# Performance work log

Hardware: AMD Instinct MI355X
Metric: run time of the kernel (lower is better)

The kernel has to match this reference:

```python
import jax, jax.numpy as jnp
import numpy as np

B, N, D, H = 2, 2048, 1024, 16
DH = D // H
DF = 4 * D
SCALE = D ** (-0.5)  # standard_scale=False -> dim**-0.5
EPS = 1e-5


def _ln(x, w, b):
    mu = jnp.mean(x, axis=-1, keepdims=True)
    var = jnp.mean(jnp.square(x - mu), axis=-1, keepdims=True)
    return (x - mu) * jax.lax.rsqrt(var + EPS) * w + b


def setup_inputs() -> dict:
    key = jax.random.key(0)
    ks = jax.random.split(key, 12)
    s = lambda fan_in: (1.0 / np.sqrt(fan_in))
    return {
        "x": jax.random.normal(ks[0], (B, N, D), jnp.float32),
        "gamma": jax.random.uniform(ks[1], (B, H), jnp.float32),
        "dist_matrix": jax.random.uniform(ks[2], (N, N), jnp.float32),
        "ln1_w": jnp.ones((D,), jnp.float32),
        "ln1_b": jnp.zeros((D,), jnp.float32),
        "qkv_w": jax.random.normal(ks[3], (D, 3 * D), jnp.float32) * s(D),
        "qkv_b": jnp.zeros((3 * D,), jnp.float32),
        "proj_w": jax.random.normal(ks[4], (D, D), jnp.float32) * s(D),
        "proj_b": jnp.zeros((D,), jnp.float32),
        "ln2_w": jnp.ones((D,), jnp.float32),
        "ln2_b": jnp.zeros((D,), jnp.float32),
        "mlp_w1": jax.random.normal(ks[5], (D, DF), jnp.float32) * s(D),
        "mlp_b1": jnp.zeros((DF,), jnp.float32),
        "mlp_w2": jax.random.normal(ks[6], (DF, D), jnp.float32) * s(DF),
        "mlp_b2": jnp.zeros((D,), jnp.float32),
    }


def reference(x, gamma, dist_matrix, ln1_w, ln1_b, qkv_w, qkv_b, proj_w, proj_b,
              ln2_w, ln2_b, mlp_w1, mlp_b1, mlp_w2, mlp_b2):
    # --- ZoomAttention on norm1(x) ---
    h = _ln(x, ln1_w, ln1_b)                                   # [B,N,D]
    qkv = h @ qkv_w + qkv_b                                    # [B,N,3D]
    qkv = qkv.reshape(B, N, 3, H, DH).transpose(2, 0, 3, 1, 4)  # [3,B,H,N,DH]
    q, k, v = qkv[0], qkv[1], qkv[2]
    scores = jnp.einsum("bhnd,bhmd->bhnm", q, k) * SCALE       # [B,H,N,N]
    scores = scores - gamma[:, :, None, None] * dist_matrix[None, None]
    attn = jax.nn.softmax(scores, axis=-1)
    out = jnp.einsum("bhnm,bhmd->bhnd", attn, v)               # [B,H,N,DH]
    out = out.transpose(0, 2, 1, 3).reshape(B, N, D)
    x = x + (out @ proj_w + proj_b)
    # --- MLP (exact GELU, torch default) ---
    h2 = _ln(x, ln2_w, ln2_b)
    h2 = jax.nn.gelu(h2 @ mlp_w1 + mlp_b1, approximate=False) @ mlp_w2 + mlp_b2
    return x + h2
```

## Files before the change

### kernel.cpp

```cpp
#include <hip/hip_runtime.h>
#include <hip/hip_bf16.h>


#define SCALE_ 0.03125f
#define EPS_   1e-5f
#define LOG2E_ 1.4426950408889634f
#define SC2_   (SCALE_ * LOG2E_)

typedef unsigned short u16;
typedef __attribute__((ext_vector_type(8))) short short8;
typedef __attribute__((ext_vector_type(4))) float f32x4;
typedef __attribute__((ext_vector_type(4))) unsigned short u16x4;

__device__ inline float b2f(u16 u){ unsigned x = ((unsigned)u) << 16; float f; __builtin_memcpy(&f, &x, 4); return f; }
__device__ inline u16 f2b(float f){ __hip_bfloat16 h = __float2bfloat16(f); u16 u; __builtin_memcpy(&u, &h, 2); return u; }

__device__ inline void glds16(const u16* g, u16* l) {
    __builtin_amdgcn_global_load_lds(
        (const __attribute__((address_space(1))) void*)g,
        (__attribute__((address_space(3))) void*)l, 16, 0, 0);
}

__global__ __launch_bounds__(256) void transpose_cast(const float* __restrict__ src,
                                                      u16* __restrict__ dst, int K, int N) {
    __shared__ float t[32][33];
    int nb = blockIdx.x * 32, kb = blockIdx.y * 32;
    int tx = threadIdx.x & 31, ty = threadIdx.x >> 5;
    for (int i = 0; i < 4; i++) {
        int r = ty + i * 8;
        t[r][tx] = src[(size_t)(kb + r) * N + nb + tx];
    }
    __syncthreads();
    for (int i = 0; i < 4; i++) {
        int r = ty + i * 8;
        dst[(size_t)(nb + r) * K + kb + tx] = f2b(t[tx][r]);
    }
}

__global__ __launch_bounds__(256) void ln_bf16(const float* __restrict__ x,
                                               const float* __restrict__ w,
                                               const float* __restrict__ b,
                                               u16* __restrict__ out) {
    int row = blockIdx.x, t = threadIdx.x;
    float4 v = ((const float4*)(x + (size_t)row * 1024))[t];
    float s1 = v.x + v.y + v.z + v.w;
    float s2 = v.x * v.x + v.y * v.y + v.z * v.z + v.w * v.w;
    for (int o = 32; o > 0; o >>= 1) { s1 += __shfl_xor(s1, o); s2 += __shfl_xor(s2, o); }
    __shared__ float a1[4], a2[4];
    if ((t & 63) == 0) { a1[t >> 6] = s1; a2[t >> 6] = s2; }
    __syncthreads();
    s1 = a1[0] + a1[1] + a1[2] + a1[3];
    s2 = a2[0] + a2[1] + a2[2] + a2[3];
    float mu = s1 * (1.0f / 1024.0f);
    float var = s2 * (1.0f / 1024.0f) - mu * mu;
    float rs = rsqrtf(var + EPS_);
    float4 wv = ((const float4*)w)[t];
    float4 bv = ((const float4*)b)[t];
    u16x4 o;
    o[0] = f2b((v.x - mu) * rs * wv.x + bv.x);
    o[1] = f2b((v.y - mu) * rs * wv.y + bv.y);
    o[2] = f2b((v.z - mu) * rs * wv.z + bv.z);
    o[3] = f2b((v.w - mu) * rs * wv.w + bv.w);
    ((u16x4*)(out + (size_t)row * 1024))[t] = o;
}

template <int MODE>
__global__ __launch_bounds__(512) void gemm256_8ph(
    const u16* __restrict__ A, const u16* __restrict__ Bt,
    const float* __restrict__ bias, int K,
    u16* __restrict__ outb,
    u16* __restrict__ qp, u16* __restrict__ kp, u16* __restrict__ vtp) {
    __shared__ u16 LS[4][2][256 * 32];
    int tid = threadIdx.x;
    int w = tid >> 6, lane = tid & 63, g = lane >> 4, ln = lane & 15;
    int wr = w >> 2, wc = w & 3;
    int gx = gridDim.x;
    int nwg = gx * gridDim.y;
    int lin = blockIdx.y * gx + blockIdx.x;
    int swz = (lin & 7) * (nwg >> 3) + (lin >> 3);
    int bx = swz % gx, by = swz / gx;
    int br = by * 256, bc = bx * 256;
    int jx = (((lane & 3) ^ ((lane >> 3) & 3)) << 3);
    const u16* Ast = A + (size_t)(br + w * 32 + (lane >> 2)) * K + jx;
    const u16* Bst = Bt + (size_t)(bc + w * 32 + (lane >> 2)) * K + jx;
    size_t r16 = (size_t)16 * K;
    const int ldsW = (w * 32) * 32;
    f32x4 acc[8][4] = {};
    int NT = K >> 5;
    int slotr = ((g ^ ((ln >> 1) & 3)) << 3);
    for (int kt = 0; kt < 3; ++kt) {
        glds16(Ast + (size_t)kt * 32, &LS[kt][0][ldsW]);
        glds16(Ast + (size_t)kt * 32 + r16, &LS[kt][0][ldsW + 512]);
        glds16(Bst + (size_t)kt * 32, &LS[kt][1][ldsW]);
        glds16(Bst + (size_t)kt * 32 + r16, &LS[kt][1][ldsW + 512]);
    }
    asm volatile("s_waitcnt vmcnt(8)" ::: "memory");
    __builtin_amdgcn_s_barrier();
    short8 aa[4], bb[4];
    for (int kt = 0; kt < NT; ++kt) {
        const u16* bufA = &LS[kt & 3][0][0];
        const u16* bufB = &LS[kt & 3][1][0];
        int s3 = kt + 3;
        #pragma unroll
        for (int m = 0; m < 4; ++m)
            aa[m] = *(const short8*)&bufA[(wr * 128 + m * 16 + ln) * 32 + slotr];
        #pragma unroll
        for (int n = 0; n < 4; ++n)
            bb[n] = *(const short8*)&bufB[(wc * 64 + n * 16 + ln) * 32 + slotr];
        if (s3 < NT) {
            u16* d = &LS[s3 & 3][0][ldsW];
            glds16(Ast + (size_t)s3 * 32, d);
            glds16(Ast + (size_t)s3 * 32 + r16, d + 512);
        }
        __builtin_amdgcn_s_barrier();
        asm volatile("s_waitcnt lgkmcnt(0)" ::: "memory");
        __builtin_amdgcn_sched_barrier(0);
        __builtin_amdgcn_s_setprio(1);
        #pragma unroll
        for (int m = 0; m < 4; ++m)
            #pragma unroll
            for (int n = 0; n < 4; ++n)
                acc[m][n] = __builtin_amdgcn_mfma_f32_16x16x32_bf16(aa[m], bb[n], acc[m][n], 0, 0, 0);
        __builtin_amdgcn_s_setprio(0);
        __builtin_amdgcn_sched_barrier(0);
        __builtin_amdgcn_s_barrier();
        #pragma unroll
        for (int m = 0; m < 4; ++m)
            aa[m] = *(const short8*)&bufA[(wr * 128 + 64 + m * 16 + ln) * 32 + slotr];
        if (s3 < NT) {
            u16* d = &LS[s3 & 3][1][ldsW];
            glds16(Bst + (size_t)s3 * 32, d);
            glds16(Bst + (size_t)s3 * 32 + r16, d + 512);
        }
        if (kt + 3 < NT)      asm volatile("s_waitcnt vmcnt(8)" ::: "memory");
        else if (kt + 2 < NT) asm volatile("s_waitcnt vmcnt(4)" ::: "memory");
        else if (kt + 1 < NT) asm volatile("s_waitcnt vmcnt(0)" ::: "memory");
        __builtin_amdgcn_s_barrier();
        asm volatile("s_waitcnt lgkmcnt(0)" ::: "memory");
        __builtin_amdgcn_sched_barrier(0);
        __builtin_amdgcn_s_setprio(1);
        #pragma unroll
        for (int m = 0; m < 4; ++m)
            #pragma unroll
            for (int n = 0; n < 4; ++n)
                acc[4 + m][n] = __builtin_amdgcn_mfma_f32_16x16x32_bf16(aa[m], bb[n], acc[4 + m][n], 0, 0, 0);
        __builtin_amdgcn_s_setprio(0);
        __builtin_amdgcn_sched_barrier(0);
        __builtin_amdgcn_s_barrier();
    }
    #pragma unroll
    for (int m = 0; m < 8; ++m) {
        int row0 = br + wr * 128 + m * 16 + g * 4;
        #pragma unroll
        for (int n = 0; n < 4; ++n) {
            int col = bc + wc * 64 + n * 16 + ln;
            float bv = bias[col];
            if constexpr (MODE == 0) {
                int which = col >> 10, cc = col & 1023, hh = cc >> 6, dh = cc & 63;
                int bb2 = row0 >> 11, nn0 = row0 & 2047;
                size_t bh = (size_t)(bb2 * 16 + hh);
                if (which == 0) {
                    for (int r = 0; r < 4; r++)
                        qp[((bh * 2048 + nn0 + r) << 6) + dh] = f2b((acc[m][n][r] + bv) * SC2_);
                } else if (which == 1) {
                    for (int r = 0; r < 4; r++)
                        kp[((bh * 2048 + nn0 + r) << 6) + dh] = f2b(acc[m][n][r] + bv);
                } else {
                    u16x4 o;
                    for (int r = 0; r < 4; r++) o[r] = f2b(acc[m][n][r] + bv);
                    *(u16x4*)&vtp[((bh * 64 + dh) << 11) + nn0] = o;
                }
            } else {
                for (int r = 0; r < 4; r++) {
                    float v = acc[m][n][r] + bv;
                    float gl = 0.5f * v * (1.0f + erff(v * 0.7071067811865476f));
                    outb[(size_t)(row0 + r) * 4096 + col] = f2b(gl);
                }
            }
        }
    }
}

template <int MODE, int BN>
__global__ __launch_bounds__(256) void gemm_bf16(
    const u16* __restrict__ A, const u16* __restrict__ Bt,
    const float* __restrict__ bias, int M, int N, int K,
    const float* __restrict__ res, float* __restrict__ outf) {
    constexpr int NN = BN / 32;
    __shared__ u16 As[128 * 64];
    __shared__ u16 Bs[BN * 64];
    int br = blockIdx.y * 128, bc = blockIdx.x * BN;
    int tid = threadIdx.x;
    int w = tid >> 6, lane = tid & 63, g = lane >> 4, ln = lane & 15;
    int wr = (w >> 1) * 64, wc = (w & 1) * (BN / 2);
    f32x4 acc[4][NN] = {};
    int sgcol = (((lane & 7) ^ (lane >> 3)) << 3);
    int arow = w * 32 + (lane >> 3);
    int brow = w * (BN / 4) + (lane >> 3);
    const u16* Ap = A + (size_t)(br + arow) * K + sgcol;
    const u16* Bp = Bt + (size_t)(bc + brow) * K + sgcol;
    u16* lA = &As[(w * 32) * 64];
    u16* lB = &Bs[(w * (BN / 4)) * 64];
    size_t rstep = (size_t)8 * K;
    for (int kt = 0; kt < K; kt += 64) {
        __syncthreads();
        #pragma unroll
        for (int i = 0; i < 4; i++) glds16(Ap + kt + i * rstep, lA + i * 512);
        #pragma unroll
        for (int i = 0; i < BN / 32; i++) glds16(Bp + kt + i * rstep, lB + i * 512);
        __syncthreads();
        #pragma unroll
        for (int kk = 0; kk < 2; kk++) {
            int so = (((kk << 2) + g) ^ (ln & 7)) << 3;
            short8 af[4], bfr[NN];
            #pragma unroll
            for (int m = 0; m < 4; m++)  af[m]  = *(const short8*)&As[(wr + m * 16 + ln) * 64 + so];
            #pragma unroll
            for (int n = 0; n < NN; n++) bfr[n] = *(const short8*)&Bs[(wc + n * 16 + ln) * 64 + so];
            #pragma unroll
            for (int m = 0; m < 4; m++)
                #pragma unroll
                for (int n = 0; n < NN; n++)
                    acc[m][n] = __builtin_amdgcn_mfma_f32_16x16x32_bf16(af[m], bfr[n], acc[m][n], 0, 0, 0);
        }
    }
    #pragma unroll
    for (int m = 0; m < 4; m++) {
        int row0 = br + wr + m * 16 + g * 4;
        #pragma unroll
        for (int n = 0; n < NN; n++) {
            int col = bc + wc + n * 16 + ln;
            float bv = bias[col];
            if constexpr (MODE == 1) {
                for (int r = 0; r < 4; r++) {
                    size_t idx = (size_t)(row0 + r) * 1024 + col;
                    outf[idx] = res[idx] + acc[m][n][r] + bv;
                }
            } else {
                for (int r = 0; r < 4; r++) {
                    size_t idx = (size_t)(row0 + r) * 1024 + col;
                    outf[idx] = outf[idx] + acc[m][n][r] + bv;
                }
            }
        }
    }
}

__global__ __launch_bounds__(256) void attn_fwd(
    const u16* __restrict__ qg, const u16* __restrict__ kg, const u16* __restrict__ vtg,
    const float* __restrict__ dist, const float* __restrict__ gamma, u16* __restrict__ ao) {
    __shared__ u16 Ks[2][64 * 64];
    __shared__ u16 Vs[2][64 * 64];
    __shared__ u16 Ps[4][16 * 64];
    int qt = blockIdx.x, bh = blockIdx.y;
    int b = bh >> 4, h = bh & 15;
    int tid = threadIdx.x, w = tid >> 6, lane = tid & 63, g = lane >> 4, ln = lane & 15;
    float gam2 = gamma[bh] * LOG2E_;
    int qglob = qt * 64 + w * 16 + ln;
    const u16* qrow = qg + ((size_t)bh * 2048 + qglob) * 64;
    short8 qf0 = *(const short8*)(qrow + g * 8);
    short8 qf1 = *(const short8*)(qrow + 32 + g * 8);
    const float* dbase = dist + (size_t)qglob * 2048 + g * 4;
    float m2 = -3.0e38f;
    f32x4 acco[4] = {};
    f32x4 accl = {};
    short8 ones;
    #pragma unroll
    for (int i = 0; i < 8; ++i) ones[i] = (short)0x3F80;
    int srow = tid >> 2, sc = (tid & 3) * 2;
    int ss0 = ((sc ^ (srow & 7)) << 3), ss1 = (((sc + 1) ^ (srow & 7)) << 3);
    const u16* kgp = kg + ((size_t)bh * 2048 + srow) * 64 + sc * 8;
    const u16* vgp = vtg + ((size_t)bh * 64 + srow) * 2048 + sc * 8;
    {
        short8 a0 = *(const short8*)(kgp);
        short8 a1 = *(const short8*)(kgp + 8);
        short8 c0 = *(const short8*)(vgp);
        short8 c1 = *(const short8*)(vgp + 8);
        *(short8*)&Ks[0][srow * 64 + ss0] = a0;
        *(short8*)&Ks[0][srow * 64 + ss1] = a1;
        *(short8*)&Vs[0][srow * 64 + ss0] = c0;
        *(short8*)&Vs[0][srow * 64 + ss1] = c1;
    }
    float4 dcv[4];
    #pragma unroll
    for (int nb = 0; nb < 4; nb++) dcv[nb] = *(const float4*)(dbase + nb * 16);
    __syncthreads();
    int cur = 0;
    int so0 = (g ^ (ln & 7)) << 3, so1 = ((4 + g) ^ (ln & 7)) << 3;
    for (int kt = 0; kt < 32; kt++) {
        short8 kr0, kr1, vr0, vr1;
        float4 dnx[4];
        if (kt < 31) {
            kr0 = *(const short8*)(kgp + (kt + 1) * 4096);
            kr1 = *(const short8*)(kgp + (kt + 1) * 4096 + 8);
            vr0 = *(const short8*)(vgp + (kt + 1) * 64);
            vr1 = *(const short8*)(vgp + (kt + 1) * 64 + 8);
            #pragma unroll
            for (int nb = 0; nb < 4; nb++)
                dnx[nb] = *(const float4*)(dbase + (kt + 1) * 64 + nb * 16);
        }
        f32x4 sa[4] = {};
        __builtin_amdgcn_s_setprio(1);
        #pragma unroll
        for (int nb = 0; nb < 4; nb++) {
            short8 kf0 = *(const short8*)&Ks[cur][(nb * 16 + ln) * 64 + so0];
            short8 kf1 = *(const short8*)&Ks[cur][(nb * 16 + ln) * 64 + so1];
            sa[nb] = __builtin_amdgcn_mfma_f32_16x16x32_bf16(kf0, qf0, sa[nb], 0, 0, 0);
            sa[nb] = __builtin_amdgcn_mfma_f32_16x16x32_bf16(kf1, qf1, sa[nb], 0, 0, 0);
        }
        __builtin_amdgcn_s_setprio(0);
        float sv[4][4], pm = -3.0e38f;
        #pragma unroll
        for (int nb = 0; nb < 4; nb++) {
            float4 dv = dcv[nb];
            sv[nb][0] = sa[nb][0] - gam2 * dv.x;
            sv[nb][1] = sa[nb][1] - gam2 * dv.y;
            sv[nb][2] = sa[nb][2] - gam2 * dv.z;
            sv[nb][3] = sa[nb][3] - gam2 * dv.w;
            #pragma unroll
            for (int r = 0; r < 4; r++) pm = fmaxf(pm, sv[nb][r]);
        }
        pm = fmaxf(pm, __shfl_xor(pm, 16));
        pm = fmaxf(pm, __shfl_xor(pm, 32));
        if (!__all(pm - m2 <= 8.0f)) {
            float nm = fmaxf(m2, pm);
            float al = __builtin_exp2f(m2 - nm);
            m2 = nm;
            accl *= al;
            #pragma unroll
            for (int db = 0; db < 4; db++) acco[db] *= al;
        }
        #pragma unroll
        for (int nb = 0; nb < 4; nb++) {
            u16x4 pw;
            #pragma unroll
            for (int r = 0; r < 4; r++) pw[r] = f2b(__builtin_exp2f(sv[nb][r] - m2));
            int off = nb * 16 + g * 4;
            *(u16x4*)&Ps[w][ln * 64 + (((off >> 3) ^ (ln & 7)) << 3) + (off & 7)] = pw;
        }
        short8 pf0 = *(const short8*)&Ps[w][ln * 64 + so0];
        short8 pf1 = *(const short8*)&Ps[w][ln * 64 + so1];
        __builtin_amdgcn_s_setprio(1);
        #pragma unroll
        for (int db = 0; db < 4; db++) {
            short8 vf0 = *(const short8*)&Vs[cur][(db * 16 + ln) * 64 + so0];
            short8 vf1 = *(const short8*)&Vs[cur][(db * 16 + ln) * 64 + so1];
            acco[db] = __builtin_amdgcn_mfma_f32_16x16x32_bf16(vf0, pf0, acco[db], 0, 0, 0);
            acco[db] = __builtin_amdgcn_mfma_f32_16x16x32_bf16(vf1, pf1, acco[db], 0, 0, 0);
        }
        accl = __builtin_amdgcn_mfma_f32_16x16x32_bf16(ones, pf0, accl, 0, 0, 0);
        accl = __builtin_amdgcn_mfma_f32_16x16x32_bf16(ones, pf1, accl, 0, 0, 0);
        __builtin_amdgcn_s_setprio(0);
        if (kt < 31) {
            int nx = cur ^ 1;
            *(short8*)&Ks[nx][srow * 64 + ss0] = kr0;
            *(short8*)&Ks[nx][srow * 64 + ss1] = kr1;
            *(short8*)&Vs[nx][srow * 64 + ss0] = vr0;
            *(short8*)&Vs[nx][srow * 64 + ss1] = vr1;
            #pragma unroll
            for (int nb = 0; nb < 4; nb++) dcv[nb] = dnx[nb];
            __syncthreads();
            cur = nx;
        }
    }
    float inv = 1.0f / accl[0];
    u16* aop = ao + (size_t)(b * 2048 + qglob) * 1024 + h * 64 + g * 4;
    #pragma unroll
    for (int db = 0; db < 4; db++) {
        u16x4 o;
        #pragma unroll
        for (int r = 0; r < 4; r++) o[r] = f2b(acco[db][r] * inv);
        *(u16x4*)(aop + db * 16) = o;
    }
}

extern "C" void kernel_launch(void* const* d_in, const int* in_sizes, int n_in,
                              void* d_out, int out_size, void* d_ws, size_t ws_size,
                              hipStream_t stream) {
    const float* x     = (const float*)d_in[0];
    const float* gamma = (const float*)d_in[1];
    const float* dist  = (const float*)d_in[2];
    const float* ln1w  = (const float*)d_in[3];
    const float* ln1b  = (const float*)d_in[4];
    const float* qkvw  = (const float*)d_in[5];
    const float* qkvb  = (const float*)d_in[6];
    const float* projw = (const float*)d_in[7];
    const float* projb = (const float*)d_in[8];
    const float* ln2w  = (const float*)d_in[9];
    const float* ln2b  = (const float*)d_in[10];
    const float* w1    = (const float*)d_in[11];
    const float* b1    = (const float*)d_in[12];
    const float* w2    = (const float*)d_in[13];
    const float* b2    = (const float*)d_in[14];
    float* out = (float*)d_out;
    char* ws = (char*)d_ws;
    u16* wqkvT  = (u16*)(ws + 0);
    u16* wprojT = (u16*)(ws + 6291456);
    u16* w1T    = (u16*)(ws + 8388608);
    u16* w2T    = (u16*)(ws + 16777216);
    u16* hb     = (u16*)(ws + 33554432);
    u16* qb     = (u16*)(ws + 41943040);
    u16* kb     = (u16*)(ws + 50331648);
    u16* vtb    = (u16*)(ws + 58720256);
    u16* aob    = (u16*)(ws + 67108864);
    u16* gb     = hb;
    u16* h2b    = aob;

    dim3 blk(256);
    transpose_cast<<<dim3(3072 / 32, 1024 / 32), blk, 0, stream>>>(qkvw, wqkvT, 1024, 3072);
    transpose_cast<<<dim3(1024 / 32, 1024 / 32), blk, 0, stream>>>(projw, wprojT, 1024, 1024);
    transpose_cast<<<dim3(4096 / 32, 1024 / 32), blk, 0, stream>>>(w1, w1T, 1024, 4096);
    transpose_cast<<<dim3(1024 / 32, 4096 / 32), blk, 0, stream>>>(w2, w2T, 4096, 1024);
    ln_bf16<<<4096, blk, 0, stream>>>(x, ln1w, ln1b, hb);
    gemm256_8ph<0><<<dim3(12, 16), dim3(512), 0, stream>>>(hb, wqkvT, qkvb, 1024,
                                                           nullptr, qb, kb, vtb);
    attn_fwd<<<dim3(32, 32), blk, 0, stream>>>(qb, kb, vtb, dist, gamma, aob);
    gemm_bf16<1, 64><<<dim3(16, 32), blk, 0, stream>>>(aob, wprojT, projb, 4096, 1024, 1024,
                                                       x, out);
    ln_bf16<<<4096, blk, 0, stream>>>(out, ln2w, ln2b, h2b);
    gemm256_8ph<2><<<dim3(16, 16), dim3(512), 0, stream>>>(h2b, w1T, b1, 1024,
                                                           gb, nullptr, nullptr, nullptr);
    gemm_bf16<3, 64><<<dim3(16, 32), blk, 0, stream>>>(gb, w2T, b2, 4096, 1024, 4096,
                                                       nullptr, out);
}
```

Measured before the change: 297.2 us.

## Rewrite attention with 32x32 MFMA, register-resident P, async LDS loads, bf16 dist

The attention kernel now gives each wave 32 query rows and uses 32x32x16 bf16 MFMA instead of 16x16x32. The softmax probabilities stay in registers, repacked with cvt_pk_bf16 and permlane32_swap, so the LDS round trip through Ps and the ones-MFMA row sum are gone. The row sum is accumulated in scalar registers instead. K and V tiles are copied with global_load_lds straight into shared memory rather than staged through registers. A new pre-pass casts the distance matrix to bf16 with log2e folded in, halving the per-tile distance traffic at the cost of an extra kernel and lower precision in the bias term.

```diff
diff --git a/kernel.cpp b/kernel.cpp
--- a/kernel.cpp
+++ b/kernel.cpp
@@ -10,6 +10,7 @@
 typedef unsigned short u16;
 typedef __attribute__((ext_vector_type(8))) short short8;
 typedef __attribute__((ext_vector_type(4))) float f32x4;
+typedef __attribute__((ext_vector_type(16))) float f32x16;
 typedef __attribute__((ext_vector_type(4))) unsigned short u16x4;
 
 __device__ inline float b2f(u16 u){ unsigned x = ((unsigned)u) << 16; float f; __builtin_memcpy(&f, &x, 4); return f; }
@@ -19,6 +20,20 @@
     __builtin_amdgcn_global_load_lds(
         (const __attribute__((address_space(1))) void*)g,
         (__attribute__((address_space(3))) void*)l, 16, 0, 0);
+}
+
+__device__ inline unsigned cvtpk(float a, float b) {
+    unsigned r;
+    asm("v_cvt_pk_bf16_f32 %0, %1, %2" : "=v"(r) : "v"(a), "v"(b));
+    return r;
+}
+__device__ inline void pl32swap(unsigned &a, unsigned &b) {
+    asm("v_permlane32_swap_b32 %0, %1" : "+v"(a), "+v"(b));
+}
+__device__ inline short8 mk8(unsigned a, unsigned b, unsigned c, unsigned d) {
+    union { unsigned u[4]; short8 s; } x;
+    x.u[0] = a; x.u[1] = b; x.u[2] = c; x.u[3] = d;
+    return x.s;
 }
 
 __global__ __launch_bounds__(256) void transpose_cast(const float* __restrict__ src,
@@ -34,6 +49,18 @@
     for (int i = 0; i < 4; i++) {
         int r = ty + i * 8;
         dst[(size_t)(nb + r) * K + kb + tx] = f2b(t[tx][r]);
+    }
+}
+
+__global__ __launch_bounds__(256) void cast_scale_bf16(const float* __restrict__ src,
+                                                       u16* __restrict__ dst, int n4, float scale) {
+    int i = blockIdx.x * 256 + threadIdx.x;
+    if (i < n4) {
+        float4 v = ((const float4*)src)[i];
+        u16x4 o;
+        o[0] = f2b(v.x * scale); o[1] = f2b(v.y * scale);
+        o[2] = f2b(v.z * scale); o[3] = f2b(v.w * scale);
+        ((u16x4*)dst)[i] = o;
     }
 }
 
@@ -246,131 +273,126 @@
     }
 }
 
-__global__ __launch_bounds__(256) void attn_fwd(
+__global__ __launch_bounds__(256) void attn_fwd32(
     const u16* __restrict__ qg, const u16* __restrict__ kg, const u16* __restrict__ vtg,
-    const float* __restrict__ dist, const float* __restrict__ gamma, u16* __restrict__ ao) {
+    const u16* __restrict__ distb, const float* __restrict__ gamma, u16* __restrict__ ao) {
     __shared__ u16 Ks[2][64 * 64];
     __shared__ u16 Vs[2][64 * 64];
-    __shared__ u16 Ps[4][16 * 64];
     int qt = blockIdx.x, bh = blockIdx.y;
-    int b = bh >> 4, h = bh & 15;
-    int tid = threadIdx.x, w = tid >> 6, lane = tid & 63, g = lane >> 4, ln = lane & 15;
-    float gam2 = gamma[bh] * LOG2E_;
-    int qglob = qt * 64 + w * 16 + ln;
+    int b = bh >> 4, h16 = bh & 15;
+    int tid = threadIdx.x, w = tid >> 6, lane = tid & 63;
+    int ln = lane & 31, hh = lane >> 5;
+    float gam = gamma[bh];
+    int qglob = qt * 128 + w * 32 + ln;
     const u16* qrow = qg + ((size_t)bh * 2048 + qglob) * 64;
-    short8 qf0 = *(const short8*)(qrow + g * 8);
-    short8 qf1 = *(const short8*)(qrow + 32 + g * 8);
-    const float* dbase = dist + (size_t)qglob * 2048 + g * 4;
-    float m2 = -3.0e38f;
-    f32x4 acco[4] = {};
-    f32x4 accl = {};
-    short8 ones;
+    short8 qB[4];
     #pragma unroll
-    for (int i = 0; i < 8; ++i) ones[i] = (short)0x3F80;
-    int srow = tid >> 2, sc = (tid & 3) * 2;
-    int ss0 = ((sc ^ (srow & 7)) << 3), ss1 = (((sc + 1) ^ (srow & 7)) << 3);
-    const u16* kgp = kg + ((size_t)bh * 2048 + srow) * 64 + sc * 8;
-    const u16* vgp = vtg + ((size_t)bh * 64 + srow) * 2048 + sc * 8;
-    {
-        short8 a0 = *(const short8*)(kgp);
-        short8 a1 = *(const short8*)(kgp + 8);
-        short8 c0 = *(const short8*)(vgp);
-        short8 c1 = *(const short8*)(vgp + 8);
-        *(short8*)&Ks[0][srow * 64 + ss0] = a0;
-        *(short8*)&Ks[0][srow * 64 + ss1] = a1;
-        *(short8*)&Vs[0][srow * 64 + ss0] = c0;
-        *(short8*)&Vs[0][srow * 64 + ss1] = c1;
-    }
-    float4 dcv[4];
-    #pragma unroll
-    for (int nb = 0; nb < 4; nb++) dcv[nb] = *(const float4*)(dbase + nb * 16);
+    for (int st = 0; st < 4; ++st) qB[st] = *(const short8*)(qrow + st * 16 + hh * 8);
+    const u16* drow = distb + (size_t)qglob * 2048 + hh * 4;
+    int srow = w * 16 + (lane >> 3);
+    int sgc = (((lane & 7) ^ ((lane >> 3) & 7)) << 3);
+    const u16* kst = kg + ((size_t)bh * 2048 + srow) * 64 + sgc;
+    const u16* vst = vtg + ((size_t)bh * 64 + srow) * 2048 + sgc;
+    u16* lk0 = &Ks[0][(w * 16) * 64]; u16* lk1 = &Ks[1][(w * 16) * 64];
+    u16* lv0 = &Vs[0][(w * 16) * 64]; u16* lv1 = &Vs[1][(w * 16) * 64];
+    glds16(kst, lk0); glds16(kst + 512, lk0 + 512);
+    glds16(vst, lv0); glds16(vst + 16384, lv0 + 512);
     __syncthreads();
+    float m2 = -3.0e38f, lsum = 0.0f;
+    f32x16 acc0 = {}, acc1 = {};
     int cur = 0;
-    int so0 = (g ^ (ln & 7)) << 3, so1 = ((4 + g) ^ (ln & 7)) << 3;
-    for (int kt = 0; kt < 32; kt++) {
-        short8 kr0, kr1, vr0, vr1;
-        float4 dnx[4];
+    for (int kt = 0; kt < 32; ++kt) {
         if (kt < 31) {
-            kr0 = *(const short8*)(kgp + (kt + 1) * 4096);
-            kr1 = *(const short8*)(kgp + (kt + 1) * 4096 + 8);
-            vr0 = *(const short8*)(vgp + (kt + 1) * 64);
-            vr1 = *(const short8*)(vgp + (kt + 1) * 64 + 8);
-            #pragma unroll
-            for (int nb = 0; nb < 4; nb++)
-                dnx[nb] = *(const float4*)(dbase + (kt + 1) * 64 + nb * 16);
-        }
-        f32x4 sa[4] = {};
+            u16* dk = cur ? lk0 : lk1;
+            u16* dvp = cur ? lv0 : lv1;
+            const u16* ks = kst + (size_t)(kt + 1) * 4096;
+            const u16* vs = vst + (size_t)(kt + 1) * 64;
+            glds16(ks, dk); glds16(ks + 512, dk + 512);
+            glds16(vs, dvp); glds16(vs + 16384, dvp + 512);
+        }
+        u16x4 dd[8];
+        #pragma unroll
+        for (int i = 0; i < 8; ++i)
+            dd[i] = *(const u16x4*)(drow + kt * 64 + (i >> 2) * 32 + (i & 3) * 8);
+        const u16* KB = &Ks[cur][0];
+        const u16* VB = &Vs[cur][0];
+        f32x16 sa0 = {}, sa1 = {};
         __builtin_amdgcn_s_setprio(1);
         #pragma unroll
-        for (int nb = 0; nb < 4; nb++) {
-            short8 kf0 = *(const short8*)&Ks[cur][(nb * 16 + ln) * 64 + so0];
-            short8 kf1 = *(const short8*)&Ks[cur][(nb * 16 + ln) * 64 + so1];
-            sa[nb] = __builtin_amdgcn_mfma_f32_16x16x32_bf16(kf0, qf0, sa[nb], 0, 0, 0);
-            sa[nb] = __builtin_amdgcn_mfma_f32_16x16x32_bf16(kf1, qf1, sa[nb], 0, 0, 0);
+        for (int st = 0; st < 4; ++st) {
+            int so = (((st * 2 + hh) ^ (ln & 7)) << 3);
+            short8 kf0 = *(const short8*)&KB[ln * 64 + so];
+            short8 kf1 = *(const short8*)&KB[(32 + ln) * 64 + so];
+            sa0 = __builtin_amdgcn_mfma_f32_32x32x16_bf16(kf0, qB[st], sa0, 0, 0, 0);
+            sa1 = __builtin_amdgcn_mfma_f32_32x32x16_bf16(kf1, qB[st], sa1, 0, 0, 0);
         }
         __builtin_amdgcn_s_setprio(0);
-        float sv[4][4], pm = -3.0e38f;
-        #pragma unroll
-        for (int nb = 0; nb < 4; nb++) {
-            float4 dv = dcv[nb];
-            sv[nb][0] = sa[nb][0] - gam2 * dv.x;
-            sv[nb][1] = sa[nb][1] - gam2 * dv.y;
-            sv[nb][2] = sa[nb][2] - gam2 * dv.z;
-            sv[nb][3] = sa[nb][3] - gam2 * dv.w;
-            #pragma unroll
-            for (int r = 0; r < 4; r++) pm = fmaxf(pm, sv[nb][r]);
-        }
-        pm = fmaxf(pm, __shfl_xor(pm, 16));
+        float p0[16], p1[16];
+        float pm = -3.0e38f;
+        #pragma unroll
+        for (int r = 0; r < 16; ++r) {
+            p0[r] = sa0[r] - gam * b2f(dd[r >> 2][r & 3]);
+            p1[r] = sa1[r] - gam * b2f(dd[4 + (r >> 2)][r & 3]);
+            pm = fmaxf(pm, fmaxf(p0[r], p1[r]));
+        }
         pm = fmaxf(pm, __shfl_xor(pm, 32));
         if (!__all(pm - m2 <= 8.0f)) {
             float nm = fmaxf(m2, pm);
             float al = __builtin_exp2f(m2 - nm);
             m2 = nm;
-            accl *= al;
-            #pragma unroll
-            for (int db = 0; db < 4; db++) acco[db] *= al;
-        }
-        #pragma unroll
-        for (int nb = 0; nb < 4; nb++) {
-            u16x4 pw;
-            #pragma unroll
-            for (int r = 0; r < 4; r++) pw[r] = f2b(__builtin_exp2f(sv[nb][r] - m2));
-            int off = nb * 16 + g * 4;
-            *(u16x4*)&Ps[w][ln * 64 + (((off >> 3) ^ (ln & 7)) << 3) + (off & 7)] = pw;
-        }
-        short8 pf0 = *(const short8*)&Ps[w][ln * 64 + so0];
-        short8 pf1 = *(const short8*)&Ps[w][ln * 64 + so1];
+            lsum *= al;
+            acc0 *= al; acc1 *= al;
+        }
+        float ps = 0.0f;
+        #pragma unroll
+        for (int r = 0; r < 16; ++r) {
+            p0[r] = __builtin_exp2f(p0[r] - m2); ps += p0[r];
+            p1[r] = __builtin_exp2f(p1[r] - m2); ps += p1[r];
+        }
+        lsum += ps;
+        unsigned w0[8], w1[8];
+        #pragma unroll
+        for (int qr = 0; qr < 4; ++qr) {
+            w0[qr * 2]     = cvtpk(p0[qr * 4], p0[qr * 4 + 1]);
+            w0[qr * 2 + 1] = cvtpk(p0[qr * 4 + 2], p0[qr * 4 + 3]);
+            w1[qr * 2]     = cvtpk(p1[qr * 4], p1[qr * 4 + 1]);
+            w1[qr * 2 + 1] = cvtpk(p1[qr * 4 + 2], p1[qr * 4 + 3]);
+        }
+        pl32swap(w0[0], w0[2]); pl32swap(w0[1], w0[3]);
+        pl32swap(w0[4], w0[6]); pl32swap(w0[5], w0[7]);
+        pl32swap(w1[0], w1[2]); pl32swap(w1[1], w1[3]);
+        pl32swap(w1[4], w1[6]); pl32swap(w1[5], w1[7]);
+        short8 pB[4];
+        pB[0] = mk8(w0[0], w0[1], w0[2], w0[3]);
+        pB[1] = mk8(w0[4], w0[5], w0[6], w0[7]);
+        pB[2] = mk8(w1[0], w1[1], w1[2], w1[3]);
+        pB[3] = mk8(w1[4], w1[5], w1[6], w1[7]);
         __builtin_amdgcn_s_setprio(1);
         #pragma unroll
-        for (int db = 0; db < 4; db++) {
-            short8 vf0 = *(const short8*)&Vs[cur][(db * 16 + ln) * 64 + so0];
-            short8 vf1 = *(const short8*)&Vs[cur][(db * 16 + ln) * 64 + so1];
-            acco[db] = __builtin_amdgcn_mfma_f32_16x16x32_bf16(vf0, pf0, acco[db], 0, 0, 0);
-            acco[db] = __builtin_amdgcn_mfma_f32_16x16x32_bf16(vf1, pf1, acco[db], 0, 0, 0);
-        }
-        accl = __builtin_amdgcn_mfma_f32_16x16x32_bf16(ones, pf0, accl, 0, 0, 0);
-        accl = __builtin_amdgcn_mfma_f32_16x16x32_bf16(ones, pf1, accl, 0, 0, 0);
+        for (int sg = 0; sg < 4; ++sg) {
+            int so = (((sg * 2 + hh) ^ (ln & 7)) << 3);
+            short8 vf0 = *(const short8*)&VB[ln * 64 + so];
+            short8 vf1 = *(const short8*)&VB[(32 + ln) * 64 + so];
+            acc0 = __builtin_amdgcn_mfma_f32_32x32x16_bf16(vf0, pB[sg], acc0, 0, 0, 0);
+            acc1 = __builtin_amdgcn_mfma_f32_32x32x16_bf16(vf1, pB[sg], acc1, 0, 0, 0);
+        }
         __builtin_amdgcn_s_setprio(0);
-        if (kt < 31) {
-            int nx = cur ^ 1;
-            *(short8*)&Ks[nx][srow * 64 + ss0] = kr0;
-            *(short8*)&Ks[nx][srow * 64 + ss1] = kr1;
-            *(short8*)&Vs[nx][srow * 64 + ss0] = vr0;
-            *(short8*)&Vs[nx][srow * 64 + ss1] = vr1;
-            #pragma unroll
-            for (int nb = 0; nb < 4; nb++) dcv[nb] = dnx[nb];
-            __syncthreads();
-            cur = nx;
-        }
-    }
-    float inv = 1.0f / accl[0];
-    u16* aop = ao + (size_t)(b * 2048 + qglob) * 1024 + h * 64 + g * 4;
+        __syncthreads();
+        cur ^= 1;
+    }
+    lsum += __shfl_xor(lsum, 32);
+    float inv = 1.0f / lsum;
+    u16* aop = ao + ((size_t)(b * 2048 + qglob)) * 1024 + h16 * 64 + hh * 4;
     #pragma unroll
-    for (int db = 0; db < 4; db++) {
-        u16x4 o;
-        #pragma unroll
-        for (int r = 0; r < 4; r++) o[r] = f2b(acco[db][r] * inv);
-        *(u16x4*)(aop + db * 16) = o;
+    for (int qr = 0; qr < 4; ++qr) {
+        u16x4 o0, o1;
+        #pragma unroll
+        for (int r = 0; r < 4; ++r) {
+            o0[r] = f2b(acc0[qr * 4 + r] * inv);
+            o1[r] = f2b(acc1[qr * 4 + r] * inv);
+        }
+        *(u16x4*)(aop + qr * 8) = o0;
+        *(u16x4*)(aop + 32 + qr * 8) = o1;
     }
 }
 
@@ -398,6 +420,7 @@
     u16* wprojT = (u16*)(ws + 6291456);
     u16* w1T    = (u16*)(ws + 8388608);
     u16* w2T    = (u16*)(ws + 16777216);
+    u16* distb  = (u16*)(ws + 25165824);
     u16* hb     = (u16*)(ws + 33554432);
     u16* qb     = (u16*)(ws + 41943040);
     u16* kb     = (u16*)(ws + 50331648);
@@ -411,10 +434,11 @@
     transpose_cast<<<dim3(1024 / 32, 1024 / 32), blk, 0, stream>>>(projw, wprojT, 1024, 1024);
     transpose_cast<<<dim3(4096 / 32, 1024 / 32), blk, 0, stream>>>(w1, w1T, 1024, 4096);
     transpose_cast<<<dim3(1024 / 32, 4096 / 32), blk, 0, stream>>>(w2, w2T, 4096, 1024);
+    cast_scale_bf16<<<4096, blk, 0, stream>>>(dist, distb, 2048 * 2048 / 4, LOG2E_);
     ln_bf16<<<4096, blk, 0, stream>>>(x, ln1w, ln1b, hb);
     gemm256_8ph<0><<<dim3(12, 16), dim3(512), 0, stream>>>(hb, wqkvT, qkvb, 1024,
                                                            nullptr, qb, kb, vtb);
-    attn_fwd<<<dim3(32, 32), blk, 0, stream>>>(qb, kb, vtb, dist, gamma, aob);
+    attn_fwd32<<<dim3(16, 32), blk, 0, stream>>>(qb, kb, vtb, distb, gamma, aob);
     gemm_bf16<1, 64><<<dim3(16, 32), blk, 0, stream>>>(aob, wprojT, projb, 4096, 1024, 1024,
                                                        x, out);
     ln_bf16<<<4096, blk, 0, stream>>>(out, ln2w, ln2b, h2b);
```

New measurement: 304.4 us. 2.4% more time.

## Cast dist matrix to bf16, widen attention blocks, sum softmax denominator in VALU

Applied to the files above, without the earlier changes.

The distance matrix is pre-cast to bf16 with log2e folded in, so the attention kernel reads half the bytes per score tile. The attention block grows to 512 threads covering 128 query rows, which halves how often K/V tiles are loaded per query. The row-sum now uses VALU adds and shuffles instead of extra MFMAs with a ones vector, and a packed bf16 conversion instruction is used. Rounding dist to bf16 adds approximation error to the bias term, and the extra cast kernel costs a full pass over the 16MB matrix.

```diff
diff --git a/kernel.cpp b/kernel.cpp
--- a/kernel.cpp
+++ b/kernel.cpp
@@ -19,6 +19,12 @@
     __builtin_amdgcn_global_load_lds(
         (const __attribute__((address_space(1))) void*)g,
         (__attribute__((address_space(3))) void*)l, 16, 0, 0);
+}
+
+__device__ inline unsigned cvtpk(float a, float b) {
+    unsigned r;
+    asm("v_cvt_pk_bf16_f32 %0, %1, %2" : "=v"(r) : "v"(a), "v"(b));
+    return r;
 }
 
 __global__ __launch_bounds__(256) void transpose_cast(const float* __restrict__ src,
@@ -34,6 +40,18 @@
     for (int i = 0; i < 4; i++) {
         int r = ty + i * 8;
         dst[(size_t)(nb + r) * K + kb + tx] = f2b(t[tx][r]);
+    }
+}
+
+__global__ __launch_bounds__(256) void cast_scale_bf16(const float* __restrict__ src,
+                                                       u16* __restrict__ dst, int n4, float scale) {
+    int i = blockIdx.x * 256 + threadIdx.x;
+    if (i < n4) {
+        float4 v = ((const float4*)src)[i];
+        u16x4 o;
+        o[0] = f2b(v.x * scale); o[1] = f2b(v.y * scale);
+        o[2] = f2b(v.z * scale); o[3] = f2b(v.w * scale);
+        ((u16x4*)dst)[i] = o;
     }
 }
 
@@ -246,58 +264,48 @@
     }
 }
 
-__global__ __launch_bounds__(256) void attn_fwd(
+__global__ __launch_bounds__(512) void attn_fwd(
     const u16* __restrict__ qg, const u16* __restrict__ kg, const u16* __restrict__ vtg,
-    const float* __restrict__ dist, const float* __restrict__ gamma, u16* __restrict__ ao) {
+    const u16* __restrict__ distb, const float* __restrict__ gamma, u16* __restrict__ ao) {
     __shared__ u16 Ks[2][64 * 64];
     __shared__ u16 Vs[2][64 * 64];
-    __shared__ u16 Ps[4][16 * 64];
+    __shared__ u16 Ps[8][16 * 64];
     int qt = blockIdx.x, bh = blockIdx.y;
     int b = bh >> 4, h = bh & 15;
     int tid = threadIdx.x, w = tid >> 6, lane = tid & 63, g = lane >> 4, ln = lane & 15;
-    float gam2 = gamma[bh] * LOG2E_;
-    int qglob = qt * 64 + w * 16 + ln;
+    float gam = gamma[bh];
+    int qglob = qt * 128 + w * 16 + ln;
     const u16* qrow = qg + ((size_t)bh * 2048 + qglob) * 64;
     short8 qf0 = *(const short8*)(qrow + g * 8);
     short8 qf1 = *(const short8*)(qrow + 32 + g * 8);
-    const float* dbase = dist + (size_t)qglob * 2048 + g * 4;
-    float m2 = -3.0e38f;
+    const u16* dbase = distb + (size_t)qglob * 2048 + g * 4;
+    float m2 = -3.0e38f, lsum = 0.0f;
     f32x4 acco[4] = {};
-    f32x4 accl = {};
-    short8 ones;
-    #pragma unroll
-    for (int i = 0; i < 8; ++i) ones[i] = (short)0x3F80;
-    int srow = tid >> 2, sc = (tid & 3) * 2;
-    int ss0 = ((sc ^ (srow & 7)) << 3), ss1 = (((sc + 1) ^ (srow & 7)) << 3);
-    const u16* kgp = kg + ((size_t)bh * 2048 + srow) * 64 + sc * 8;
-    const u16* vgp = vtg + ((size_t)bh * 64 + srow) * 2048 + sc * 8;
+    int srow = tid >> 3, seg = tid & 7;
+    int ss = ((seg ^ (srow & 7)) << 3);
+    const u16* kgp = kg + ((size_t)bh * 2048 + srow) * 64 + seg * 8;
+    const u16* vgp = vtg + ((size_t)bh * 64 + srow) * 2048 + seg * 8;
     {
         short8 a0 = *(const short8*)(kgp);
-        short8 a1 = *(const short8*)(kgp + 8);
         short8 c0 = *(const short8*)(vgp);
-        short8 c1 = *(const short8*)(vgp + 8);
-        *(short8*)&Ks[0][srow * 64 + ss0] = a0;
-        *(short8*)&Ks[0][srow * 64 + ss1] = a1;
-        *(short8*)&Vs[0][srow * 64 + ss0] = c0;
-        *(short8*)&Vs[0][srow * 64 + ss1] = c1;
-    }
-    float4 dcv[4];
+        *(short8*)&Ks[0][srow * 64 + ss] = a0;
+        *(short8*)&Vs[0][srow * 64 + ss] = c0;
+    }
+    u16x4 dcv[4];
     #pragma unroll
-    for (int nb = 0; nb < 4; nb++) dcv[nb] = *(const float4*)(dbase + nb * 16);
+    for (int nb = 0; nb < 4; nb++) dcv[nb] = *(const u16x4*)(dbase + nb * 16);
     __syncthreads();
     int cur = 0;
     int so0 = (g ^ (ln & 7)) << 3, so1 = ((4 + g) ^ (ln & 7)) << 3;
     for (int kt = 0; kt < 32; kt++) {
-        short8 kr0, kr1, vr0, vr1;
-        float4 dnx[4];
+        short8 kr0, vr0;
+        u16x4 dnx[4];
         if (kt < 31) {
             kr0 = *(const short8*)(kgp + (kt + 1) * 4096);
-            kr1 = *(const short8*)(kgp + (kt + 1) * 4096 + 8);
             vr0 = *(const short8*)(vgp + (kt + 1) * 64);
-            vr1 = *(const short8*)(vgp + (kt + 1) * 64 + 8);
             #pragma unroll
             for (int nb = 0; nb < 4; nb++)
-                dnx[nb] = *(const float4*)(dbase + (kt + 1) * 64 + nb * 16);
+                dnx[nb] = *(const u16x4*)(dbase + (kt + 1) * 64 + nb * 16);
         }
         f32x4 sa[4] = {};
         __builtin_amdgcn_s_setprio(1);
@@ -312,13 +320,10 @@
         float sv[4][4], pm = -3.0e38f;
         #pragma unroll
         for (int nb = 0; nb < 4; nb++) {
-            float4 dv = dcv[nb];
-            sv[nb][0] = sa[nb][0] - gam2 * dv.x;
-            sv[nb][1] = sa[nb][1] - gam2 * dv.y;
-            sv[nb][2] = sa[nb][2] - gam2 * dv.z;
-            sv[nb][3] = sa[nb][3] - gam2 * dv.w;
-            #pragma unroll
-            for (int r = 0; r < 4; r++) pm = fmaxf(pm, sv[nb][r]);
+            #pragma unroll
+            for (int r = 0; r < 4; r++)
+                sv[nb][r] = sa[nb][r] - gam * b2f(dcv[nb][r]);
+            pm = fmaxf(pm, fmaxf(fmaxf(sv[nb][0], sv[nb][1]), fmaxf(sv[nb][2], sv[nb][3])));
         }
         pm = fmaxf(pm, __shfl_xor(pm, 16));
         pm = fmaxf(pm, __shfl_xor(pm, 32));
@@ -326,18 +331,27 @@
             float nm = fmaxf(m2, pm);
             float al = __builtin_exp2f(m2 - nm);
             m2 = nm;
-            accl *= al;
+            lsum *= al;
             #pragma unroll
             for (int db = 0; db < 4; db++) acco[db] *= al;
         }
+        float ps = 0.0f;
         #pragma unroll
         for (int nb = 0; nb < 4; nb++) {
-            u16x4 pw;
-            #pragma unroll
-            for (int r = 0; r < 4; r++) pw[r] = f2b(__builtin_exp2f(sv[nb][r] - m2));
+            float e0 = __builtin_exp2f(sv[nb][0] - m2);
+            float e1 = __builtin_exp2f(sv[nb][1] - m2);
+            float e2 = __builtin_exp2f(sv[nb][2] - m2);
+            float e3 = __builtin_exp2f(sv[nb][3] - m2);
+            ps += (e0 + e1) + (e2 + e3);
+            union { unsigned u[2]; u16x4 v; } pk;
+            pk.u[0] = cvtpk(e0, e1);
+            pk.u[1] = cvtpk(e2, e3);
             int off = nb * 16 + g * 4;
-            *(u16x4*)&Ps[w][ln * 64 + (((off >> 3) ^ (ln & 7)) << 3) + (off & 7)] = pw;
-        }
+            *(u16x4*)&Ps[w][ln * 64 + (((off >> 3) ^ (ln & 7)) << 3) + (off & 7)] = pk.v;
+        }
+        ps += __shfl_xor(ps, 16);
+        ps += __shfl_xor(ps, 32);
+        lsum += ps;
         short8 pf0 = *(const short8*)&Ps[w][ln * 64 + so0];
         short8 pf1 = *(const short8*)&Ps[w][ln * 64 + so1];
         __builtin_amdgcn_s_setprio(1);
@@ -348,22 +362,18 @@
             acco[db] = __builtin_amdgcn_mfma_f32_16x16x32_bf16(vf0, pf0, acco[db], 0, 0, 0);
             acco[db] = __builtin_amdgcn_mfma_f32_16x16x32_bf16(vf1, pf1, acco[db], 0, 0, 0);
         }
-        accl = __builtin_amdgcn_mfma_f32_16x16x32_bf16(ones, pf0, accl, 0, 0, 0);
-        accl = __builtin_amdgcn_mfma_f32_16x16x32_bf16(ones, pf1, accl, 0, 0, 0);
         __builtin_amdgcn_s_setprio(0);
         if (kt < 31) {
             int nx = cur ^ 1;
-            *(short8*)&Ks[nx][srow * 64 + ss0] = kr0;
-            *(short8*)&Ks[nx][srow * 64 + ss1] = kr1;
-            *(short8*)&Vs[nx][srow * 64 + ss0] = vr0;
-            *(short8*)&Vs[nx][srow * 64 + ss1] = vr1;
+            *(short8*)&Ks[nx][srow * 64 + ss] = kr0;
+            *(short8*)&Vs[nx][srow * 64 + ss] = vr0;
             #pragma unroll
             for (int nb = 0; nb < 4; nb++) dcv[nb] = dnx[nb];
             __syncthreads();
             cur = nx;
         }
     }
-    float inv = 1.0f / accl[0];
+    float inv = 1.0f / lsum;
     u16* aop = ao + (size_t)(b * 2048 + qglob) * 1024 + h * 64 + g * 4;
     #pragma unroll
     for (int db = 0; db < 4; db++) {
@@ -398,6 +408,7 @@
     u16* wprojT = (u16*)(ws + 6291456);
     u16* w1T    = (u16*)(ws + 8388608);
     u16* w2T    = (u16*)(ws + 16777216);
+    u16* distb  = (u16*)(ws + 25165824);
     u16* hb     = (u16*)(ws + 33554432);
     u16* qb     = (u16*)(ws + 41943040);
     u16* kb     = (u16*)(ws + 50331648);
@@ -411,10 +422,11 @@
     transpose_cast<<<dim3(1024 / 32, 1024 / 32), blk, 0, stream>>>(projw, wprojT, 1024, 1024);
     transpose_cast<<<dim3(4096 / 32, 1024 / 32), blk, 0, stream>>>(w1, w1T, 1024, 4096);
     transpose_cast<<<dim3(1024 / 32, 4096 / 32), blk, 0, stream>>>(w2, w2T, 4096, 1024);
+    cast_scale_bf16<<<4096, blk, 0, stream>>>(dist, distb, 2048 * 2048 / 4, LOG2E_);
     ln_bf16<<<4096, blk, 0, stream>>>(x, ln1w, ln1b, hb);
     gemm256_8ph<0><<<dim3(12, 16), dim3(512), 0, stream>>>(hb, wqkvT, qkvb, 1024,
                                                            nullptr, qb, kb, vtb);
-    attn_fwd<<<dim3(32, 32), blk, 0, stream>>>(qb, kb, vtb, dist, gamma, aob);
+    attn_fwd<<<dim3(16, 32), dim3(512), 0, stream>>>(qb, kb, vtb, distb, gamma, aob);
     gemm_bf16<1, 64><<<dim3(16, 32), blk, 0, stream>>>(aob, wprojT, projb, 4096, 1024, 1024,
                                                        x, out);
     ln_bf16<<<4096, blk, 0, stream>>>(out, ln2w, ln2b, h2b);
```

After: 282.9 us. 4.8% less time.
